# Optimization experiments

Measured on AMD Instinct MI355X. Metric: run time of the kernel, lower is better.

Reference implementation:

```python
import jax, jax.numpy as jnp
import numpy as np

H = 1024      # hidden_size
L = 128       # max_length
V = 50257     # output_size (vocab)


def setup_inputs() -> dict:
    key = jax.random.key(0)
    ks = jax.random.split(key, 16)
    s = 1.0 / np.sqrt(H)
    inp = {
        "x": jax.random.randint(ks[0], (1,), 0, V, dtype=jnp.int64)
        if jax.config.jax_enable_x64 else jax.random.randint(ks[0], (1,), 0, V, dtype=jnp.int32),
        "hidden": jax.random.normal(ks[1], (1, 1, H), dtype=jnp.float32),
        "encoder_outputs": jax.random.normal(ks[2], (L, H), dtype=jnp.float32),
        # learned parameters
        "emb": jax.random.normal(ks[3], (V, H), dtype=jnp.float32),
        "attn_W": jax.random.uniform(ks[4], (L, 2 * H), jnp.float32, -s, s),
        "attn_b": jax.random.uniform(ks[5], (L,), jnp.float32, -s, s),
        "comb_W": jax.random.uniform(ks[6], (H, 2 * H), jnp.float32, -s, s),
        "comb_b": jax.random.uniform(ks[7], (H,), jnp.float32, -s, s),
        "W_ih": jax.random.uniform(ks[8], (3 * H, H), jnp.float32, -s, s),
        "W_hh": jax.random.uniform(ks[9], (3 * H, H), jnp.float32, -s, s),
        "b_ih": jax.random.uniform(ks[10], (3 * H,), jnp.float32, -s, s),
        "b_hh": jax.random.uniform(ks[11], (3 * H,), jnp.float32, -s, s),
        "out_W": jax.random.uniform(ks[12], (V, H), jnp.float32, -s, s),
        "out_b": jax.random.uniform(ks[13], (V,), jnp.float32, -s, s),
    }
    return inp


def _gru_cell(x_t, h, W_ih, W_hh, b_ih, b_hh):
    # PyTorch GRU gate order: r, z, n
    gx = x_t @ W_ih.T + b_ih              # [1, 3H]
    gh = h @ W_hh.T + b_hh                # [1, 3H]
    gx_r, gx_z, gx_n = jnp.split(gx, 3, axis=1)
    gh_r, gh_z, gh_n = jnp.split(gh, 3, axis=1)
    r = jax.nn.sigmoid(gx_r + gh_r)
    z = jax.nn.sigmoid(gx_z + gh_z)
    n = jnp.tanh(gx_n + r * gh_n)
    return (1.0 - z) * n + z * h          # [1, H]


def reference(x, hidden, encoder_outputs, emb, attn_W, attn_b, comb_W, comb_b,
              W_ih, W_hh, b_ih, b_hh, out_W, out_b):
    embedded = emb[x]                                        # [1, H]
    h0 = hidden[0]                                           # [1, H]
    cat_eh = jnp.concatenate([embedded, h0], axis=1)         # [1, 2H]
    attention_weights = jax.nn.softmax(cat_eh @ attn_W.T + attn_b, axis=1)  # [1, L]
    with_attention = attention_weights @ encoder_outputs     # [1, H]
    combined = jnp.concatenate([embedded, with_attention], axis=1)  # [1, 2H]
    rnn_in = jax.nn.relu(combined @ comb_W.T + comb_b)       # [1, H]
    h_new = _gru_cell(rnn_in, h0, W_ih, W_hh, b_ih, b_hh)    # [1, H]
    logp = jax.nn.log_softmax(h_new @ out_W.T + out_b, axis=1)  # [1, V]
    return logp, h_new[None, :, :], attention_weights
```

## Files before the change

### kernel.cpp

```cpp
#include <hip/hip_runtime.h>
#include <math.h>

#define H 1024
#define L 128
#define V 50257
#define NB6 2048

#define WS_AL    0
#define WS_WATT  128
#define WS_RNN   (128+1024)
#define WS_GX    (128+2048)
#define WS_GH    (128+2048+3072)
#define WS_HNEW  (128+2048+6144)
#define WS_PM    (128+2048+6144+1024)
#define WS_PS    (WS_PM + NB6)
#define WS_LSE   (WS_PS + NB6)

__device__ __forceinline__ float wred(float v) {
    v += __shfl_down(v, 32);
    v += __shfl_down(v, 16);
    v += __shfl_down(v, 8);
    v += __shfl_down(v, 4);
    v += __shfl_down(v, 2);
    v += __shfl_down(v, 1);
    return v;
}

__global__ __launch_bounds__(256) void k_attn_logits(
        const float* __restrict__ emb, const int* __restrict__ x,
        const float* __restrict__ hid, const float* __restrict__ attn_W,
        const float* __restrict__ attn_b, float* __restrict__ ws) {
    int wave = blockIdx.x * 4 + (threadIdx.x >> 6);
    int lane = threadIdx.x & 63;
    const float* er = emb + (size_t)x[0] * H;
    const float* w  = attn_W + (size_t)wave * (2 * H);
    float acc = 0.f;
    #pragma unroll
    for (int k = 0; k < 8; ++k) {
        int j = (k * 64 + lane) * 4;
        float4 wv = *(const float4*)(w + j);
        const float* src = (j < H) ? (er + j) : (hid + (j - H));
        float4 cv = *(const float4*)src;
        acc += wv.x * cv.x + wv.y * cv.y + wv.z * cv.z + wv.w * cv.w;
    }
    acc = wred(acc);
    if (lane == 0) ws[WS_AL + wave] = acc + attn_b[wave];
}

__global__ __launch_bounds__(256) void k_attn_apply(
        const float* __restrict__ enc, float* __restrict__ ws,
        float* __restrict__ out) {
    __shared__ float sl[L];
    __shared__ float swt[L];
    int t = threadIdx.x;
    if (t < L) sl[t] = ws[WS_AL + t];
    __syncthreads();
    float m = -1e30f;
    #pragma unroll 8
    for (int i = 0; i < L; ++i) m = fmaxf(m, sl[i]);
    float s = 0.f;
    #pragma unroll 4
    for (int i = 0; i < L; ++i) s += expf(sl[i] - m);
    float inv = 1.f / s;
    if (t < L) swt[t] = expf(sl[t] - m) * inv;
    __syncthreads();
    int h = blockIdx.x * 256 + t;
    float acc = 0.f;
    #pragma unroll 8
    for (int l = 0; l < L; ++l) acc += swt[l] * enc[l * H + h];
    ws[WS_WATT + h] = acc;
    if (blockIdx.x == 0 && t < L) out[V + H + t] = swt[t];
}

__global__ __launch_bounds__(256) void k_rnn_gh(
        const float* __restrict__ emb, const int* __restrict__ x,
        const float* __restrict__ hid, const float* __restrict__ comb_W,
        const float* __restrict__ comb_b, const float* __restrict__ W_hh,
        const float* __restrict__ b_hh, float* __restrict__ ws) {
    int wave = blockIdx.x * 4 + (threadIdx.x >> 6);
    int lane = threadIdx.x & 63;
    if (wave < H) {
        const float* er = emb + (size_t)x[0] * H;
        const float* w  = comb_W + (size_t)wave * (2 * H);
        const float* watt = ws + WS_WATT;
        float acc = 0.f;
        #pragma unroll
        for (int k = 0; k < 8; ++k) {
            int j = (k * 64 + lane) * 4;
            float4 wv = *(const float4*)(w + j);
            const float* src = (j < H) ? (er + j) : (watt + (j - H));
            float4 cv = *(const float4*)src;
            acc += wv.x * cv.x + wv.y * cv.y + wv.z * cv.z + wv.w * cv.w;
        }
        acc = wred(acc);
        if (lane == 0) ws[WS_RNN + wave] = fmaxf(acc + comb_b[wave], 0.f);
    } else {
        int r = wave - H;
        const float* w = W_hh + (size_t)r * H;
        float acc = 0.f;
        #pragma unroll
        for (int k = 0; k < 4; ++k) {
            int j = (k * 64 + lane) * 4;
            float4 wv = *(const float4*)(w + j);
            float4 hv = *(const float4*)(hid + j);
            acc += wv.x * hv.x + wv.y * hv.y + wv.z * hv.z + wv.w * hv.w;
        }
        acc = wred(acc);
        if (lane == 0) ws[WS_GH + r] = acc + b_hh[r];
    }
}

__global__ __launch_bounds__(256) void k_gx(
        const float* __restrict__ W_ih, const float* __restrict__ b_ih,
        float* __restrict__ ws) {
    int r = blockIdx.x * 4 + (threadIdx.x >> 6);
    int lane = threadIdx.x & 63;
    const float* w = W_ih + (size_t)r * H;
    const float* rn = ws + WS_RNN;
    float acc = 0.f;
    #pragma unroll
    for (int k = 0; k < 4; ++k) {
        int j = (k * 64 + lane) * 4;
        float4 wv = *(const float4*)(w + j);
        float4 rv = *(const float4*)(rn + j);
        acc += wv.x * rv.x + wv.y * rv.y + wv.z * rv.z + wv.w * rv.w;
    }
    acc = wred(acc);
    if (lane == 0) ws[WS_GX + r] = acc + b_ih[r];
}

__global__ __launch_bounds__(256) void k_gru(
        const float* __restrict__ hid, float* __restrict__ ws,
        float* __restrict__ out) {
    int h = blockIdx.x * 256 + threadIdx.x;
    const float* gx = ws + WS_GX;
    const float* gh = ws + WS_GH;
    float r = 1.f / (1.f + expf(-(gx[h] + gh[h])));
    float z = 1.f / (1.f + expf(-(gx[H + h] + gh[H + h])));
    float n = tanhf(gx[2 * H + h] + r * gh[2 * H + h]);
    float hn = (1.f - z) * n + z * hid[h];
    ws[WS_HNEW + h] = hn;
    out[V + h] = hn;
}

__global__ __launch_bounds__(256) void k_logits(
        const float* __restrict__ out_W, const float* __restrict__ out_b,
        float* __restrict__ ws, float* __restrict__ out) {
    int wid = threadIdx.x >> 6;
    int lane = threadIdx.x & 63;
    int gw = blockIdx.x * 4 + wid;
    const float* hn = ws + WS_HNEW;
    float m = -INFINITY, s = 0.f;
    for (int row = gw; row < V; row += NB6 * 4) {
        const float* w = out_W + (size_t)row * H;
        float acc = 0.f;
        #pragma unroll
        for (int k = 0; k < 4; ++k) {
            int j = (k * 64 + lane) * 4;
            float4 wv = *(const float4*)(w + j);
            float4 hv = *(const float4*)(hn + j);
            acc += wv.x * hv.x + wv.y * hv.y + wv.z * hv.z + wv.w * hv.w;
        }
        acc = wred(acc);
        if (lane == 0) {
            float logit = acc + out_b[row];
            out[row] = logit;
            if (logit > m) { s = s * expf(m - logit) + 1.f; m = logit; }
            else           { s += expf(logit - m); }
        }
    }
    __shared__ float sm[4], ss[4];
    if (lane == 0) { sm[wid] = m; ss[wid] = s; }
    __syncthreads();
    if (threadIdx.x == 0) {
        float M = fmaxf(fmaxf(sm[0], sm[1]), fmaxf(sm[2], sm[3]));
        float S = ss[0] * expf(sm[0] - M) + ss[1] * expf(sm[1] - M)
                + ss[2] * expf(sm[2] - M) + ss[3] * expf(sm[3] - M);
        ws[WS_PM + blockIdx.x] = M;
        ws[WS_PS + blockIdx.x] = S;
    }
}

__global__ __launch_bounds__(256) void k_lse(float* __restrict__ ws) {
    __shared__ float sm[256], ss[256];
    int t = threadIdx.x;
    float m = -INFINITY, s = 0.f;
    for (int i = t; i < NB6; i += 256) {
        float mi = ws[WS_PM + i], si = ws[WS_PS + i];
        float M = fmaxf(m, mi);
        s = s * expf(m - M) + si * expf(mi - M);
        m = M;
    }
    sm[t] = m; ss[t] = s;
    __syncthreads();
    for (int off = 128; off > 0; off >>= 1) {
        if (t < off) {
            float m2 = sm[t + off], s2 = ss[t + off];
            float M = fmaxf(sm[t], m2);
            ss[t] = ss[t] * expf(sm[t] - M) + s2 * expf(m2 - M);
            sm[t] = M;
        }
        __syncthreads();
    }
    if (t == 0) ws[WS_LSE] = sm[0] + logf(ss[0]);
}

__global__ __launch_bounds__(256) void k_finalize(
        float* __restrict__ out, const float* __restrict__ ws) {
    int i = blockIdx.x * 256 + threadIdx.x;
    if (i < V) out[i] -= ws[WS_LSE];
}

extern "C" void kernel_launch(void* const* d_in, const int* in_sizes, int n_in,
                              void* d_out, int out_size, void* d_ws, size_t ws_size,
                              hipStream_t stream) {
    const int*   x      = (const int*)  d_in[0];
    const float* hidden = (const float*)d_in[1];
    const float* enc    = (const float*)d_in[2];
    const float* emb    = (const float*)d_in[3];
    const float* attn_W = (const float*)d_in[4];
    const float* attn_b = (const float*)d_in[5];
    const float* comb_W = (const float*)d_in[6];
    const float* comb_b = (const float*)d_in[7];
    const float* W_ih   = (const float*)d_in[8];
    const float* W_hh   = (const float*)d_in[9];
    const float* b_ih   = (const float*)d_in[10];
    const float* b_hh   = (const float*)d_in[11];
    const float* out_W  = (const float*)d_in[12];
    const float* out_b  = (const float*)d_in[13];
    float* out = (float*)d_out;
    float* ws  = (float*)d_ws;

    k_attn_logits<<<32, 256, 0, stream>>>(emb, x, hidden, attn_W, attn_b, ws);
    k_attn_apply <<<4, 256, 0, stream>>>(enc, ws, out);
    k_rnn_gh     <<<1024, 256, 0, stream>>>(emb, x, hidden, comb_W, comb_b, W_hh, b_hh, ws);
    k_gx         <<<768, 256, 0, stream>>>(W_ih, b_ih, ws);
    k_gru        <<<4, 256, 0, stream>>>(hidden, ws, out);
    k_logits     <<<NB6, 256, 0, stream>>>(out_W, out_b, ws, out);
    k_lse        <<<1, 256, 0, stream>>>(ws);
    k_finalize   <<<(V + 255) / 256, 256, 0, stream>>>(out, ws);
}
```

Before: 439.1 us.

## Fuse kernels: move W_hh GEMV into attention stage, GRU into logits, LSE into finalize

Moves the W_hh·h GEMV, which depends only on the input hidden state, into the first attention-logits kernel. It also folds the GRU gate computation into every logits block, which keeps h_new in shared memory, and merges the LSE reduction into each finalize block. This cuts the launch count from eight to six. The attention-apply step is split across 16 blocks with a 4-way partial sum over L for more parallelism. The cost is redundant work: every logits block recomputes the GRU, and every finalize block re-reduces the 2048 partials.

Measured after the change: 432.6 us. Within noise of the previous version (-1.5%).

```diff
diff --git a/kernel.cpp b/kernel.cpp
--- a/kernel.cpp
+++ b/kernel.cpp
@@ -11,10 +11,8 @@
 #define WS_RNN   (128+1024)
 #define WS_GX    (128+2048)
 #define WS_GH    (128+2048+3072)
-#define WS_HNEW  (128+2048+6144)
-#define WS_PM    (128+2048+6144+1024)
+#define WS_PM    (128+2048+6144)
 #define WS_PS    (WS_PM + NB6)
-#define WS_LSE   (WS_PS + NB6)
 
 __device__ __forceinline__ float wred(float v) {
     v += __shfl_down(v, 32);
@@ -26,25 +24,41 @@
     return v;
 }
 
-__global__ __launch_bounds__(256) void k_attn_logits(
+__global__ __launch_bounds__(256) void k_attn_gh(
         const float* __restrict__ emb, const int* __restrict__ x,
         const float* __restrict__ hid, const float* __restrict__ attn_W,
-        const float* __restrict__ attn_b, float* __restrict__ ws) {
-    int wave = blockIdx.x * 4 + (threadIdx.x >> 6);
+        const float* __restrict__ attn_b, const float* __restrict__ W_hh,
+        const float* __restrict__ b_hh, float* __restrict__ ws) {
+    int w = blockIdx.x * 4 + (threadIdx.x >> 6);
     int lane = threadIdx.x & 63;
-    const float* er = emb + (size_t)x[0] * H;
-    const float* w  = attn_W + (size_t)wave * (2 * H);
-    float acc = 0.f;
-    #pragma unroll
-    for (int k = 0; k < 8; ++k) {
-        int j = (k * 64 + lane) * 4;
-        float4 wv = *(const float4*)(w + j);
-        const float* src = (j < H) ? (er + j) : (hid + (j - H));
-        float4 cv = *(const float4*)src;
-        acc += wv.x * cv.x + wv.y * cv.y + wv.z * cv.z + wv.w * cv.w;
-    }
-    acc = wred(acc);
-    if (lane == 0) ws[WS_AL + wave] = acc + attn_b[wave];
+    if (w < L) {
+        const float* er = emb + (size_t)x[0] * H;
+        const float* aw = attn_W + (size_t)w * (2 * H);
+        float acc = 0.f;
+        #pragma unroll
+        for (int k = 0; k < 8; ++k) {
+            int j = (k * 64 + lane) * 4;
+            float4 wv = *(const float4*)(aw + j);
+            const float* src = (j < H) ? (er + j) : (hid + (j - H));
+            float4 cv = *(const float4*)src;
+            acc += wv.x * cv.x + wv.y * cv.y + wv.z * cv.z + wv.w * cv.w;
+        }
+        acc = wred(acc);
+        if (lane == 0) ws[WS_AL + w] = acc + attn_b[w];
+    } else {
+        int r = w - L;
+        const float* wr = W_hh + (size_t)r * H;
+        float acc = 0.f;
+        #pragma unroll
+        for (int k = 0; k < 4; ++k) {
+            int j = (k * 64 + lane) * 4;
+            float4 wv = *(const float4*)(wr + j);
+            float4 hv = *(const float4*)(hid + j);
+            acc += wv.x * hv.x + wv.y * hv.y + wv.z * hv.z + wv.w * hv.w;
+        }
+        acc = wred(acc);
+        if (lane == 0) ws[WS_GH + r] = acc + b_hh[r];
+    }
 }
 
 __global__ __launch_bounds__(256) void k_attn_apply(
@@ -52,6 +66,7 @@
         float* __restrict__ out) {
     __shared__ float sl[L];
     __shared__ float swt[L];
+    __shared__ float part[4][64];
     int t = threadIdx.x;
     if (t < L) sl[t] = ws[WS_AL + t];
     __syncthreads();
@@ -64,50 +79,38 @@
     float inv = 1.f / s;
     if (t < L) swt[t] = expf(sl[t] - m) * inv;
     __syncthreads();
-    int h = blockIdx.x * 256 + t;
+    int col = t & 63, q = t >> 6;
+    int h = blockIdx.x * 64 + col;
     float acc = 0.f;
     #pragma unroll 8
-    for (int l = 0; l < L; ++l) acc += swt[l] * enc[l * H + h];
-    ws[WS_WATT + h] = acc;
+    for (int l = q * 32; l < q * 32 + 32; ++l) acc += swt[l] * enc[l * H + h];
+    part[q][col] = acc;
+    __syncthreads();
+    if (q == 0)
+        ws[WS_WATT + h] = part[0][col] + part[1][col] + part[2][col] + part[3][col];
     if (blockIdx.x == 0 && t < L) out[V + H + t] = swt[t];
 }
 
-__global__ __launch_bounds__(256) void k_rnn_gh(
+__global__ __launch_bounds__(256) void k_rnn_in(
         const float* __restrict__ emb, const int* __restrict__ x,
-        const float* __restrict__ hid, const float* __restrict__ comb_W,
-        const float* __restrict__ comb_b, const float* __restrict__ W_hh,
-        const float* __restrict__ b_hh, float* __restrict__ ws) {
+        const float* __restrict__ comb_W, const float* __restrict__ comb_b,
+        float* __restrict__ ws) {
     int wave = blockIdx.x * 4 + (threadIdx.x >> 6);
     int lane = threadIdx.x & 63;
-    if (wave < H) {
-        const float* er = emb + (size_t)x[0] * H;
-        const float* w  = comb_W + (size_t)wave * (2 * H);
-        const float* watt = ws + WS_WATT;
-        float acc = 0.f;
-        #pragma unroll
-        for (int k = 0; k < 8; ++k) {
-            int j = (k * 64 + lane) * 4;
-            float4 wv = *(const float4*)(w + j);
-            const float* src = (j < H) ? (er + j) : (watt + (j - H));
-            float4 cv = *(const float4*)src;
-            acc += wv.x * cv.x + wv.y * cv.y + wv.z * cv.z + wv.w * cv.w;
-        }
-        acc = wred(acc);
-        if (lane == 0) ws[WS_RNN + wave] = fmaxf(acc + comb_b[wave], 0.f);
-    } else {
-        int r = wave - H;
-        const float* w = W_hh + (size_t)r * H;
-        float acc = 0.f;
-        #pragma unroll
-        for (int k = 0; k < 4; ++k) {
-            int j = (k * 64 + lane) * 4;
-            float4 wv = *(const float4*)(w + j);
-            float4 hv = *(const float4*)(hid + j);
-            acc += wv.x * hv.x + wv.y * hv.y + wv.z * hv.z + wv.w * hv.w;
-        }
-        acc = wred(acc);
-        if (lane == 0) ws[WS_GH + r] = acc + b_hh[r];
-    }
+    const float* er = emb + (size_t)x[0] * H;
+    const float* w  = comb_W + (size_t)wave * (2 * H);
+    const float* watt = ws + WS_WATT;
+    float acc = 0.f;
+    #pragma unroll
+    for (int k = 0; k < 8; ++k) {
+        int j = (k * 64 + lane) * 4;
+        float4 wv = *(const float4*)(w + j);
+        const float* src = (j < H) ? (er + j) : (watt + (j - H));
+        float4 cv = *(const float4*)src;
+        acc += wv.x * cv.x + wv.y * cv.y + wv.z * cv.z + wv.w * cv.w;
+    }
+    acc = wred(acc);
+    if (lane == 0) ws[WS_RNN + wave] = fmaxf(acc + comb_b[wave], 0.f);
 }
 
 __global__ __launch_bounds__(256) void k_gx(
@@ -129,27 +132,28 @@
     if (lane == 0) ws[WS_GX + r] = acc + b_ih[r];
 }
 
-__global__ __launch_bounds__(256) void k_gru(
+__global__ __launch_bounds__(256) void k_logits(
+        const float* __restrict__ out_W, const float* __restrict__ out_b,
         const float* __restrict__ hid, float* __restrict__ ws,
         float* __restrict__ out) {
-    int h = blockIdx.x * 256 + threadIdx.x;
+    __shared__ float sh[H];
+    int t = threadIdx.x;
     const float* gx = ws + WS_GX;
     const float* gh = ws + WS_GH;
-    float r = 1.f / (1.f + expf(-(gx[h] + gh[h])));
-    float z = 1.f / (1.f + expf(-(gx[H + h] + gh[H + h])));
-    float n = tanhf(gx[2 * H + h] + r * gh[2 * H + h]);
-    float hn = (1.f - z) * n + z * hid[h];
-    ws[WS_HNEW + h] = hn;
-    out[V + h] = hn;
-}
-
-__global__ __launch_bounds__(256) void k_logits(
-        const float* __restrict__ out_W, const float* __restrict__ out_b,
-        float* __restrict__ ws, float* __restrict__ out) {
-    int wid = threadIdx.x >> 6;
-    int lane = threadIdx.x & 63;
+    #pragma unroll
+    for (int i = t; i < H; i += 256) {
+        float r = 1.f / (1.f + expf(-(gx[i] + gh[i])));
+        float z = 1.f / (1.f + expf(-(gx[H + i] + gh[H + i])));
+        float n = tanhf(gx[2 * H + i] + r * gh[2 * H + i]);
+        float hn = (1.f - z) * n + z * hid[i];
+        sh[i] = hn;
+        if (blockIdx.x == 0) out[V + i] = hn;
+    }
+    __syncthreads();
+
+    int wid = t >> 6;
+    int lane = t & 63;
     int gw = blockIdx.x * 4 + wid;
-    const float* hn = ws + WS_HNEW;
     float m = -INFINITY, s = 0.f;
     for (int row = gw; row < V; row += NB6 * 4) {
         const float* w = out_W + (size_t)row * H;
@@ -158,7 +162,7 @@
         for (int k = 0; k < 4; ++k) {
             int j = (k * 64 + lane) * 4;
             float4 wv = *(const float4*)(w + j);
-            float4 hv = *(const float4*)(hn + j);
+            float4 hv = *(const float4*)(sh + j);
             acc += wv.x * hv.x + wv.y * hv.y + wv.z * hv.z + wv.w * hv.w;
         }
         acc = wred(acc);
@@ -172,7 +176,7 @@
     __shared__ float sm[4], ss[4];
     if (lane == 0) { sm[wid] = m; ss[wid] = s; }
     __syncthreads();
-    if (threadIdx.x == 0) {
+    if (t == 0) {
         float M = fmaxf(fmaxf(sm[0], sm[1]), fmaxf(sm[2], sm[3]));
         float S = ss[0] * expf(sm[0] - M) + ss[1] * expf(sm[1] - M)
                 + ss[2] * expf(sm[2] - M) + ss[3] * expf(sm[3] - M);
@@ -181,7 +185,8 @@
     }
 }
 
-__global__ __launch_bounds__(256) void k_lse(float* __restrict__ ws) {
+__global__ __launch_bounds__(256) void k_finalize(
+        float* __restrict__ out, const float* __restrict__ ws) {
     __shared__ float sm[256], ss[256];
     int t = threadIdx.x;
     float m = -INFINITY, s = 0.f;
@@ -202,13 +207,9 @@
         }
         __syncthreads();
     }
-    if (t == 0) ws[WS_LSE] = sm[0] + logf(ss[0]);
-}
-
-__global__ __launch_bounds__(256) void k_finalize(
-        float* __restrict__ out, const float* __restrict__ ws) {
-    int i = blockIdx.x * 256 + threadIdx.x;
-    if (i < V) out[i] -= ws[WS_LSE];
+    float lse = sm[0] + logf(ss[0]);
+    int i = blockIdx.x * 256 + t;
+    if (i < V) out[i] -= lse;
 }
 
 extern "C" void kernel_launch(void* const* d_in, const int* in_sizes, int n_in,
@@ -231,12 +232,10 @@
     float* out = (float*)d_out;
     float* ws  = (float*)d_ws;
 
-    k_attn_logits<<<32, 256, 0, stream>>>(emb, x, hidden, attn_W, attn_b, ws);
-    k_attn_apply <<<4, 256, 0, stream>>>(enc, ws, out);
-    k_rnn_gh     <<<1024, 256, 0, stream>>>(emb, x, hidden, comb_W, comb_b, W_hh, b_hh, ws);
+    k_attn_gh    <<<800, 256, 0, stream>>>(emb, x, hidden, attn_W, attn_b, W_hh, b_hh, ws);
+    k_attn_apply <<<16, 256, 0, stream>>>(enc, ws, out);
+    k_rnn_in     <<<256, 256, 0, stream>>>(emb, x, comb_W, comb_b, ws);
     k_gx         <<<768, 256, 0, stream>>>(W_ih, b_ih, ws);
-    k_gru        <<<4, 256, 0, stream>>>(hidden, ws, out);
-    k_logits     <<<NB6, 256, 0, stream>>>(out_W, out_b, ws, out);
-    k_lse        <<<1, 256, 0, stream>>>(ws);
+    k_logits     <<<NB6, 256, 0, stream>>>(out_W, out_b, hidden, ws, out);
     k_finalize   <<<(V + 255) / 256, 256, 0, stream>>>(out, ws);
 }
```
